# Kernel tuning notes

Measured on AMD Instinct MI355X. Metric: run time of the kernel, lower is better.

Reference implementation:

```python
import jax, jax.numpy as jnp
import numpy as np

B, N, C = 16, 2048, 512
NUM_HEADS = 8
D = C // NUM_HEADS  # 64


def setup_inputs() -> dict:
    key = jax.random.key(0)
    ks = jax.random.split(key, 8)
    s = 0.02
    return {
        "x": jax.random.normal(ks[0], (B, N, C), dtype=jnp.float32),
        "Wq": jax.random.normal(ks[1], (D, C), dtype=jnp.float32) * s,
        "bq": jax.random.normal(ks[2], (D,), dtype=jnp.float32) * s,
        "Wk": jax.random.normal(ks[3], (D, C), dtype=jnp.float32) * s,
        "bk": jax.random.normal(ks[4], (D,), dtype=jnp.float32) * s,
        "Wv": jax.random.normal(ks[5], (C, C), dtype=jnp.float32) * s,
        "bv": jax.random.normal(ks[6], (C,), dtype=jnp.float32) * s,
        "gamma": jax.random.normal(ks[7], (1,), dtype=jnp.float32) * 0.1,
    }


def reference(x, Wq, bq, Wk, bk, Wv, bv, gamma):
    # x: [B, N, C]; torch code permutes to [B, C, N] (channels for Conv1d)
    xt = jnp.transpose(x, (0, 2, 1))                      # [B, C, N]
    # 1x1 Conv1d == pointwise linear over channel dim
    q = jnp.einsum('dc,bcn->bdn', Wq, xt) + bq[None, :, None]   # [B, D, N]
    k = jnp.einsum('dc,bcn->bdn', Wk, xt) + bk[None, :, None]   # [B, D, N]
    v = jnp.einsum('oc,bcn->bon', Wv, xt) + bv[None, :, None]   # [B, C, N]
    # energy[b, n, m] = <q[:, n], k[:, m]>
    energy = jnp.einsum('bdn,bdm->bnm', q, k)             # [B, N, N]
    attention = jax.nn.softmax(energy, axis=-1)           # [B, N, N]
    # out = bmm(v, attention^T): out[b, c, n] = sum_m v[b, c, m] * attn[b, n, m]
    out = jnp.einsum('bcm,bnm->bcn', v, attention)        # [B, C, N]
    out = gamma[0] * out + xt
    return jnp.transpose(out, (0, 2, 1))                  # [B, N, C]
```

## Files before the change

### kernel.cpp

```cpp
#include <hip/hip_runtime.h>
#include <hip/hip_bf16.h>

typedef __bf16 bf16x8 __attribute__((ext_vector_type(8)));
typedef float f32x4 __attribute__((ext_vector_type(4)));

#define B_ 16
#define N_ 2048
#define C_ 512
#define D_ 64

__device__ __forceinline__ float bf2f(ushort u) {
    union { uint i; float f; } w; w.i = ((uint)u) << 16; return w.f;
}
__device__ __forceinline__ ushort f2bf(float f) {
    union { float f; uint i; } w; w.f = f;
    uint u = w.i;
    u = (u + 0x7fffu + ((u >> 16) & 1u)) >> 16;
    return (ushort)u;
}
__device__ __forceinline__ __bf16 u2b(ushort u) {
    union { ushort s; __bf16 b; } w; w.s = u; return w.b;
}
__device__ __forceinline__ bf16x8 ld8u(const ushort* p) { return *(const bf16x8*)p; }
__device__ __forceinline__ bf16x8 ld8f(const float* p) {
    f32x4 a = *(const f32x4*)p;
    f32x4 b = *(const f32x4*)(p + 4);
    bf16x8 r;
    r[0] = u2b(f2bf(a[0])); r[1] = u2b(f2bf(a[1]));
    r[2] = u2b(f2bf(a[2])); r[3] = u2b(f2bf(a[3]));
    r[4] = u2b(f2bf(b[0])); r[5] = u2b(f2bf(b[1]));
    r[6] = u2b(f2bf(b[2])); r[7] = u2b(f2bf(b[3]));
    return r;
}

__device__ __forceinline__ void gload16(const ushort* g, ushort* l) {
    __builtin_amdgcn_global_load_lds(
        (const __attribute__((address_space(1))) void*)g,
        (__attribute__((address_space(3))) void*)l, 16, 0, 0);
}

__global__ void probe_kernel(const void* x, int* flag) {
    int lane = threadIdx.x & 63;
    ushort u = ((const ushort*)x)[lane * 2];
    float v = fabsf(bf2f(u));
    bool sane = (v > 9.3e-10f) && (v < 1.1e9f) && (v == v);
    unsigned long long m = __ballot(sane);
    if (threadIdx.x == 0) *flag = (__popcll(m) >= 48) ? 0 : 1;
}

__launch_bounds__(256, 2)
__global__ void proj_qk_kernel(const void* __restrict__ X,
                               const void* __restrict__ Wq_,
                               const void* __restrict__ bq_,
                               const void* __restrict__ Wk_,
                               const void* __restrict__ bk_,
                               ushort* __restrict__ outq,
                               ushort* __restrict__ outk,
                               const int* __restrict__ flag) {
    const int isf32 = *flag;
    const ushort* Xu  = (const ushort*)X;
    const float*  Xf  = (const float*)X;
    const ushort* Wqu = (const ushort*)Wq_;
    const float*  Wqf = (const float*)Wq_;
    const ushort* Wku = (const ushort*)Wk_;
    const float*  Wkf = (const float*)Wk_;
    const ushort* Bqu = (const ushort*)bq_;
    const float*  Bqf = (const float*)bq_;
    const ushort* Bku = (const ushort*)bk_;
    const float*  Bkf = (const float*)bk_;

    __shared__ ushort lA[64][72];
    __shared__ ushort lBq[64][72];
    __shared__ ushort lBk[64][72];
    const int tid  = threadIdx.x;
    const int wave = tid >> 6, lane = tid & 63;
    const int quad = lane >> 4, li = lane & 15;
    const int m0 = blockIdx.x * 64;

    f32x4 accq[4], acck[4];
    #pragma unroll
    for (int t = 0; t < 4; ++t) {
        accq[t] = (f32x4){0.f, 0.f, 0.f, 0.f};
        acck[t] = (f32x4){0.f, 0.f, 0.f, 0.f};
    }

    for (int k0 = 0; k0 < C_; k0 += 64) {
        __syncthreads();
        #pragma unroll
        for (int it = 0; it < 2; ++it) {
            int idx = tid + it * 256;
            int row = idx >> 3, seg = idx & 7;
            size_t ea = (size_t)(m0 + row) * C_ + k0 + seg * 8;
            size_t eb = (size_t)row * C_ + k0 + seg * 8;
            if (!isf32) {
                *(bf16x8*)&lA[row][seg * 8]  = ld8u(Xu + ea);
                *(bf16x8*)&lBq[row][seg * 8] = ld8u(Wqu + eb);
                *(bf16x8*)&lBk[row][seg * 8] = ld8u(Wku + eb);
            } else {
                *(bf16x8*)&lA[row][seg * 8]  = ld8f(Xf + ea);
                *(bf16x8*)&lBq[row][seg * 8] = ld8f(Wqf + eb);
                *(bf16x8*)&lBk[row][seg * 8] = ld8f(Wkf + eb);
            }
        }
        __syncthreads();
        #pragma unroll
        for (int ks = 0; ks < 2; ++ks) {
            bf16x8 a = *(const bf16x8*)&lA[wave * 16 + li][ks * 32 + quad * 8];
            #pragma unroll
            for (int t = 0; t < 4; ++t) {
                bf16x8 bq8 = *(const bf16x8*)&lBq[t * 16 + li][ks * 32 + quad * 8];
                bf16x8 bk8 = *(const bf16x8*)&lBk[t * 16 + li][ks * 32 + quad * 8];
                accq[t] = __builtin_amdgcn_mfma_f32_16x16x32_bf16(a, bq8, accq[t], 0, 0, 0);
                acck[t] = __builtin_amdgcn_mfma_f32_16x16x32_bf16(a, bk8, acck[t], 0, 0, 0);
            }
        }
    }

    #pragma unroll
    for (int t = 0; t < 4; ++t) {
        int c = t * 16 + li;
        float bvq = isf32 ? Bqf[c] : bf2f(Bqu[c]);
        float bvk = isf32 ? Bkf[c] : bf2f(Bku[c]);
        #pragma unroll
        for (int j = 0; j < 4; ++j) {
            int m = m0 + wave * 16 + quad * 4 + j;
            outq[(size_t)m * D_ + c] = f2bf(accq[t][j] + bvq);
            outk[(size_t)m * D_ + c] = f2bf(acck[t][j] + bvk);
        }
    }
}

template<int NCOLS, int MODE>
__launch_bounds__(256, 2)
__global__ void proj_kernel(const void* __restrict__ X,
                            const void* __restrict__ W,
                            const void* __restrict__ bias,
                            ushort* __restrict__ out,
                            const int* __restrict__ flag,
                            size_t xoff) {
    const int isf32 = *flag;
    const ushort* Xu = (const ushort*)X + xoff;
    const float*  Xf = (const float*)X + xoff;
    const ushort* Wu = (const ushort*)W;
    const float*  Wf = (const float*)W;
    const ushort* Bu = (const ushort*)bias;
    const float*  Bf = (const float*)bias;

    __shared__ ushort lA[64][72];
    __shared__ ushort lB[64][72];
    const int tid  = threadIdx.x;
    const int wave = tid >> 6, lane = tid & 63;
    const int quad = lane >> 4, li = lane & 15;
    const int m0 = blockIdx.x * 64;
    const int n0 = blockIdx.y * 64;

    f32x4 acc[4];
    #pragma unroll
    for (int t = 0; t < 4; ++t) acc[t] = (f32x4){0.f, 0.f, 0.f, 0.f};

    for (int k0 = 0; k0 < C_; k0 += 64) {
        __syncthreads();
        #pragma unroll
        for (int it = 0; it < 2; ++it) {
            int idx = tid + it * 256;
            int row = idx >> 3, seg = idx & 7;
            size_t ea = (size_t)(m0 + row) * C_ + k0 + seg * 8;
            size_t eb = (size_t)(n0 + row) * C_ + k0 + seg * 8;
            if (!isf32) {
                *(bf16x8*)&lA[row][seg * 8] = ld8u(Xu + ea);
                *(bf16x8*)&lB[row][seg * 8] = ld8u(Wu + eb);
            } else {
                *(bf16x8*)&lA[row][seg * 8] = ld8f(Xf + ea);
                *(bf16x8*)&lB[row][seg * 8] = ld8f(Wf + eb);
            }
        }
        __syncthreads();
        #pragma unroll
        for (int ks = 0; ks < 2; ++ks) {
            bf16x8 a = *(const bf16x8*)&lA[wave * 16 + li][ks * 32 + quad * 8];
            #pragma unroll
            for (int t = 0; t < 4; ++t) {
                bf16x8 b = *(const bf16x8*)&lB[t * 16 + li][ks * 32 + quad * 8];
                acc[t] = __builtin_amdgcn_mfma_f32_16x16x32_bf16(a, b, acc[t], 0, 0, 0);
            }
        }
    }

    #pragma unroll
    for (int t = 0; t < 4; ++t) {
        int c = n0 + t * 16 + li;
        float bv = isf32 ? Bf[c] : bf2f(Bu[c]);
        if (MODE == 0) {
            #pragma unroll
            for (int j = 0; j < 4; ++j) {
                int m = m0 + wave * 16 + quad * 4 + j;
                out[(size_t)m * NCOLS + c] = f2bf(acc[t][j] + bv);
            }
        } else {
            int m = m0 + wave * 16 + quad * 4;
            int b = m >> 11, ml = m & (N_ - 1);
            ushort4 pk;
            pk.x = f2bf(acc[t][0] + bv);
            pk.y = f2bf(acc[t][1] + bv);
            pk.z = f2bf(acc[t][2] + bv);
            pk.w = f2bf(acc[t][3] + bv);
            *(ushort4*)(out + ((size_t)(b * C_ + c)) * N_ + ml) = pk;
        }
    }
}

__launch_bounds__(512, 4)
__global__ void attn_fused(const ushort* __restrict__ q,
                           const ushort* __restrict__ kk,
                           const ushort* __restrict__ vt,
                           const void* __restrict__ x,
                           const void* __restrict__ gptr,
                           void* __restrict__ out,
                           const int* __restrict__ flag) {
    __shared__ ushort Vl[2][256 * 64];
    __shared__ ushort Pl[64 * 64];
    __shared__ float  ll[64];

    const int tid  = threadIdx.x;
    const int wave = tid >> 6, lane = tid & 63;
    const int quad = lane >> 4, li = lane & 15;
    const int wq = wave & 1;
    const int wm = wave >> 1;
    const int b  = blockIdx.z;
    const int q0 = blockIdx.x * 64;
    const int c0 = blockIdx.y * 256;

    const ushort* kb = kk + (size_t)b * N_ * D_;
    const ushort* vb = vt + ((size_t)b * C_ + c0) * N_;

    const int lrow8 = lane >> 3;
    const int lseg  = (lane & 7) ^ lrow8;

    bf16x8 qf[2][2];
    #pragma unroll
    for (int i = 0; i < 2; ++i)
        #pragma unroll
        for (int ks = 0; ks < 2; ++ks)
            qf[i][ks] = ld8u(q + ((size_t)(b * N_ + q0 + wq * 32 + i * 16 + li)) * D_
                               + ks * 32 + quad * 8);

    f32x4 acc[2][4];
    #pragma unroll
    for (int i = 0; i < 2; ++i)
        #pragma unroll
        for (int j = 0; j < 4; ++j) acc[i][j] = (f32x4){0.f, 0.f, 0.f, 0.f};

    f32x4 accp[2];
    float s4[2][4];
    #pragma unroll
    for (int i = 0; i < 2; ++i) {
        accp[i] = (f32x4){0.f, 0.f, 0.f, 0.f};
        #pragma unroll
        for (int j = 0; j < 4; ++j) s4[i][j] = 0.f;
    }

    #pragma unroll
    for (int it = 0; it < 4; ++it) {
        int rbase = wave * 32 + it * 8;
        gload16(vb + (size_t)(rbase + lrow8) * N_ + lseg * 8, &Vl[0][rbase * 64]);
    }
    {
        bf16x8 k0 = ld8u(kb + (size_t)(wm * 16 + li) * D_ + quad * 8);
        bf16x8 k1 = ld8u(kb + (size_t)(wm * 16 + li) * D_ + 32 + quad * 8);
        accp[0] = __builtin_amdgcn_mfma_f32_16x16x32_bf16(qf[0][0], k0, accp[0], 0, 0, 0);
        accp[1] = __builtin_amdgcn_mfma_f32_16x16x32_bf16(qf[1][0], k0, accp[1], 0, 0, 0);
        accp[0] = __builtin_amdgcn_mfma_f32_16x16x32_bf16(qf[0][1], k1, accp[0], 0, 0, 0);
        accp[1] = __builtin_amdgcn_mfma_f32_16x16x32_bf16(qf[1][1], k1, accp[1], 0, 0, 0);
    }
    bf16x8 kreg0 = ld8u(kb + (size_t)(64 + wm * 16 + li) * D_ + quad * 8);
    bf16x8 kreg1 = ld8u(kb + (size_t)(64 + wm * 16 + li) * D_ + 32 + quad * 8);

    for (int t = 0; t < 32; ++t) {
        const int cur = t & 1;
        if (t < 31) {
            #pragma unroll
            for (int it = 0; it < 4; ++it) {
                int rbase = wave * 32 + it * 8;
                gload16(vb + (size_t)(rbase + lrow8) * N_ + (t + 1) * 64 + lseg * 8,
                        &Vl[cur ^ 1][rbase * 64]);
            }
        }
        #pragma unroll
        for (int i = 0; i < 2; ++i)
            #pragma unroll
            for (int j = 0; j < 4; ++j) {
                int r = wq * 32 + i * 16 + quad * 4 + j;
                int m = wm * 16 + li;
                float e = __expf(fminf(accp[i][j], 60.f));
                s4[i][j] += e;
                *(__bf16*)&Pl[r * 64 + (((m >> 3) ^ (r & 7)) * 8) + (m & 7)] = (__bf16)e;
            }
        if (t < 31) {
            f32x4 np0 = (f32x4){0.f, 0.f, 0.f, 0.f};
            f32x4 np1 = (f32x4){0.f, 0.f, 0.f, 0.f};
            np0 = __builtin_amdgcn_mfma_f32_16x16x32_bf16(qf[0][0], kreg0, np0, 0, 0, 0);
            np1 = __builtin_amdgcn_mfma_f32_16x16x32_bf16(qf[1][0], kreg0, np1, 0, 0, 0);
            np0 = __builtin_amdgcn_mfma_f32_16x16x32_bf16(qf[0][1], kreg1, np0, 0, 0, 0);
            np1 = __builtin_amdgcn_mfma_f32_16x16x32_bf16(qf[1][1], kreg1, np1, 0, 0, 0);
            if (t < 30) {
                kreg0 = ld8u(kb + (size_t)((t + 2) * 64 + wm * 16 + li) * D_ + quad * 8);
                kreg1 = ld8u(kb + (size_t)((t + 2) * 64 + wm * 16 + li) * D_ + 32 + quad * 8);
            }
            accp[0] = np0;
            accp[1] = np1;
        }
        if (t < 30)       asm volatile("s_waitcnt vmcnt(6) lgkmcnt(0)" ::: "memory");
        else if (t == 30) asm volatile("s_waitcnt vmcnt(4) lgkmcnt(0)" ::: "memory");
        else              asm volatile("s_waitcnt vmcnt(0) lgkmcnt(0)" ::: "memory");
        __builtin_amdgcn_sched_barrier(0);
        __builtin_amdgcn_s_barrier();
        __builtin_amdgcn_sched_barrier(0);

        __builtin_amdgcn_s_setprio(1);
        #pragma unroll
        for (int ks = 0; ks < 2; ++ks) {
            bf16x8 af[2];
            #pragma unroll
            for (int i = 0; i < 2; ++i)
                af[i] = *(const bf16x8*)&Pl[(wq * 32 + i * 16 + li) * 64
                                            + (((ks * 4 + quad) ^ (li & 7)) * 8)];
            #pragma unroll
            for (int j = 0; j < 4; ++j) {
                bf16x8 vf = *(const bf16x8*)&Vl[cur][(wm * 64 + j * 16 + li) * 64
                                                    + (((ks * 4 + quad) ^ (li & 7)) * 8)];
                #pragma unroll
                for (int i = 0; i < 2; ++i)
                    acc[i][j] = __builtin_amdgcn_mfma_f32_16x16x32_bf16(
                        af[i], vf, acc[i][j], 0, 0, 0);
            }
        }
        __builtin_amdgcn_s_setprio(0);

        __builtin_amdgcn_sched_barrier(0);
        __builtin_amdgcn_s_barrier();
        __builtin_amdgcn_sched_barrier(0);
    }

    __syncthreads();
    if (tid < 64) ll[tid] = 0.f;
    __syncthreads();
    #pragma unroll
    for (int i = 0; i < 2; ++i)
        #pragma unroll
        for (int j = 0; j < 4; ++j) {
            float s = s4[i][j];
            s += __shfl_xor(s, 1, 64);
            s += __shfl_xor(s, 2, 64);
            s += __shfl_xor(s, 4, 64);
            s += __shfl_xor(s, 8, 64);
            if (li == 0) atomicAdd(&ll[wq * 32 + i * 16 + quad * 4 + j], s);
        }
    __syncthreads();

    const int isf32 = *flag;
    const float g = isf32 ? ((const float*)gptr)[0] : bf2f(((const ushort*)gptr)[0]);
    const ushort* xu = (const ushort*)x;
    const float*  xf = (const float*)x;
    ushort* ou = (ushort*)out;
    float*  of = (float*)out;
    #pragma unroll
    for (int i = 0; i < 2; ++i)
        #pragma unroll
        for (int jj = 0; jj < 4; ++jj) {
            int nl = wq * 32 + i * 16 + quad * 4 + jj;
            float inv = 1.f / ll[nl];
            size_t rowb = ((size_t)(b * N_ + q0 + nl)) * C_;
            #pragma unroll
            for (int j = 0; j < 4; ++j) {
                int cg = c0 + wm * 64 + j * 16 + li;
                size_t idx = rowb + cg;
                float xv  = isf32 ? xf[idx] : bf2f(xu[idx]);
                float val = g * (acc[i][j][jj] * inv) + xv;
                if (isf32) of[idx] = val; else ou[idx] = f2bf(val);
            }
        }
}

extern "C" void kernel_launch(void* const* d_in, const int* in_sizes, int n_in,
                              void* d_out, int out_size, void* d_ws, size_t ws_size,
                              hipStream_t stream) {
    (void)in_sizes; (void)n_in; (void)out_size; (void)ws_size;
    const void* x     = d_in[0];
    const void* Wq    = d_in[1];
    const void* bq    = d_in[2];
    const void* Wk    = d_in[3];
    const void* bk    = d_in[4];
    const void* Wv    = d_in[5];
    const void* bv    = d_in[6];
    const void* gamma = d_in[7];

    int*    flag = (int*)d_ws;
    ushort* q    = (ushort*)((char*)d_ws + 256);
    ushort* kk   = q  + (size_t)B_ * N_ * D_;
    ushort* vt   = kk + (size_t)B_ * N_ * D_;

    probe_kernel<<<1, 64, 0, stream>>>(x, flag);

    const int M = B_ * N_;
    proj_qk_kernel<<<dim3(M / 64), 256, 0, stream>>>(x, Wq, bq, Wk, bk, q, kk, flag);
    proj_kernel<C_, 1><<<dim3(M / 64, C_ / 64), 256, 0, stream>>>(
        x, Wv, bv, vt, flag, 0);
    attn_fused<<<dim3(N_ / 64, 2, B_), 512, 0, stream>>>(
        q, kk, vt, x, gamma, d_out, flag);
}
```

Before: 330.1 us.

## Merge Q/K/V projections into one 128x128-tiled GEMM kernel

Replaces the separate QK and V projection kernels with a single GEMM over the concatenated 640-column weight (Wq|Wk|Wv). Each block now computes a 128x128 tile with 2x2 waves and 4x4 MFMA fragments per wave, so each A and B fragment loaded from LDS is reused more often, and x is read fewer times overall. The epilogue sends each column to the q, k or transposed v output. In exchange it uses more registers and LDS per block, adds per-row branches in the weight-load address selection, and the q/k stores stay scalar and uncoalesced.

```diff
diff --git a/kernel.cpp b/kernel.cpp
--- a/kernel.cpp
+++ b/kernel.cpp
@@ -49,162 +49,108 @@
 }
 
 __launch_bounds__(256, 2)
-__global__ void proj_qk_kernel(const void* __restrict__ X,
-                               const void* __restrict__ Wq_,
-                               const void* __restrict__ bq_,
-                               const void* __restrict__ Wk_,
-                               const void* __restrict__ bk_,
-                               ushort* __restrict__ outq,
-                               ushort* __restrict__ outk,
-                               const int* __restrict__ flag) {
+__global__ void proj_all(const void* __restrict__ X,
+                         const void* __restrict__ Wq_, const void* __restrict__ bq_,
+                         const void* __restrict__ Wk_, const void* __restrict__ bk_,
+                         const void* __restrict__ Wv_, const void* __restrict__ bv_,
+                         ushort* __restrict__ outq,
+                         ushort* __restrict__ outk,
+                         ushort* __restrict__ outv,
+                         const int* __restrict__ flag) {
     const int isf32 = *flag;
-    const ushort* Xu  = (const ushort*)X;
-    const float*  Xf  = (const float*)X;
-    const ushort* Wqu = (const ushort*)Wq_;
-    const float*  Wqf = (const float*)Wq_;
-    const ushort* Wku = (const ushort*)Wk_;
-    const float*  Wkf = (const float*)Wk_;
-    const ushort* Bqu = (const ushort*)bq_;
-    const float*  Bqf = (const float*)bq_;
-    const ushort* Bku = (const ushort*)bk_;
-    const float*  Bkf = (const float*)bk_;
-
-    __shared__ ushort lA[64][72];
-    __shared__ ushort lBq[64][72];
-    __shared__ ushort lBk[64][72];
+    __shared__ ushort lA[128][72];
+    __shared__ ushort lB[128][72];
     const int tid  = threadIdx.x;
     const int wave = tid >> 6, lane = tid & 63;
     const int quad = lane >> 4, li = lane & 15;
-    const int m0 = blockIdx.x * 64;
-
-    f32x4 accq[4], acck[4];
-    #pragma unroll
-    for (int t = 0; t < 4; ++t) {
-        accq[t] = (f32x4){0.f, 0.f, 0.f, 0.f};
-        acck[t] = (f32x4){0.f, 0.f, 0.f, 0.f};
-    }
+    const int wr = (wave & 1) * 64;
+    const int wc = (wave >> 1) * 64;
+    const int m0 = blockIdx.x * 128;
+    const int n0 = blockIdx.y * 128;
+
+    f32x4 acc[4][4];
+    #pragma unroll
+    for (int i = 0; i < 4; ++i)
+        #pragma unroll
+        for (int j = 0; j < 4; ++j) acc[i][j] = (f32x4){0.f, 0.f, 0.f, 0.f};
 
     for (int k0 = 0; k0 < C_; k0 += 64) {
         __syncthreads();
         #pragma unroll
-        for (int it = 0; it < 2; ++it) {
+        for (int it = 0; it < 4; ++it) {
             int idx = tid + it * 256;
             int row = idx >> 3, seg = idx & 7;
+            int n = n0 + row;
             size_t ea = (size_t)(m0 + row) * C_ + k0 + seg * 8;
-            size_t eb = (size_t)row * C_ + k0 + seg * 8;
             if (!isf32) {
-                *(bf16x8*)&lA[row][seg * 8]  = ld8u(Xu + ea);
-                *(bf16x8*)&lBq[row][seg * 8] = ld8u(Wqu + eb);
-                *(bf16x8*)&lBk[row][seg * 8] = ld8u(Wku + eb);
+                const ushort* bs = (n < 64)  ? (const ushort*)Wq_ + (size_t)n * C_
+                                 : (n < 128) ? (const ushort*)Wk_ + (size_t)(n - 64) * C_
+                                             : (const ushort*)Wv_ + (size_t)(n - 128) * C_;
+                *(bf16x8*)&lA[row][seg * 8] = ld8u((const ushort*)X + ea);
+                *(bf16x8*)&lB[row][seg * 8] = ld8u(bs + k0 + seg * 8);
             } else {
-                *(bf16x8*)&lA[row][seg * 8]  = ld8f(Xf + ea);
-                *(bf16x8*)&lBq[row][seg * 8] = ld8f(Wqf + eb);
-                *(bf16x8*)&lBk[row][seg * 8] = ld8f(Wkf + eb);
+                const float* bs = (n < 64)  ? (const float*)Wq_ + (size_t)n * C_
+                                : (n < 128) ? (const float*)Wk_ + (size_t)(n - 64) * C_
+                                            : (const float*)Wv_ + (size_t)(n - 128) * C_;
+                *(bf16x8*)&lA[row][seg * 8] = ld8f((const float*)X + ea);
+                *(bf16x8*)&lB[row][seg * 8] = ld8f(bs + k0 + seg * 8);
             }
         }
         __syncthreads();
         #pragma unroll
         for (int ks = 0; ks < 2; ++ks) {
-            bf16x8 a = *(const bf16x8*)&lA[wave * 16 + li][ks * 32 + quad * 8];
-            #pragma unroll
-            for (int t = 0; t < 4; ++t) {
-                bf16x8 bq8 = *(const bf16x8*)&lBq[t * 16 + li][ks * 32 + quad * 8];
-                bf16x8 bk8 = *(const bf16x8*)&lBk[t * 16 + li][ks * 32 + quad * 8];
-                accq[t] = __builtin_amdgcn_mfma_f32_16x16x32_bf16(a, bq8, accq[t], 0, 0, 0);
-                acck[t] = __builtin_amdgcn_mfma_f32_16x16x32_bf16(a, bk8, acck[t], 0, 0, 0);
-            }
-        }
-    }
-
-    #pragma unroll
-    for (int t = 0; t < 4; ++t) {
-        int c = t * 16 + li;
-        float bvq = isf32 ? Bqf[c] : bf2f(Bqu[c]);
-        float bvk = isf32 ? Bkf[c] : bf2f(Bku[c]);
-        #pragma unroll
-        for (int j = 0; j < 4; ++j) {
-            int m = m0 + wave * 16 + quad * 4 + j;
-            outq[(size_t)m * D_ + c] = f2bf(accq[t][j] + bvq);
-            outk[(size_t)m * D_ + c] = f2bf(acck[t][j] + bvk);
-        }
-    }
-}
-
-template<int NCOLS, int MODE>
-__launch_bounds__(256, 2)
-__global__ void proj_kernel(const void* __restrict__ X,
-                            const void* __restrict__ W,
-                            const void* __restrict__ bias,
-                            ushort* __restrict__ out,
-                            const int* __restrict__ flag,
-                            size_t xoff) {
-    const int isf32 = *flag;
-    const ushort* Xu = (const ushort*)X + xoff;
-    const float*  Xf = (const float*)X + xoff;
-    const ushort* Wu = (const ushort*)W;
-    const float*  Wf = (const float*)W;
-    const ushort* Bu = (const ushort*)bias;
-    const float*  Bf = (const float*)bias;
-
-    __shared__ ushort lA[64][72];
-    __shared__ ushort lB[64][72];
-    const int tid  = threadIdx.x;
-    const int wave = tid >> 6, lane = tid & 63;
-    const int quad = lane >> 4, li = lane & 15;
-    const int m0 = blockIdx.x * 64;
-    const int n0 = blockIdx.y * 64;
-
-    f32x4 acc[4];
-    #pragma unroll
-    for (int t = 0; t < 4; ++t) acc[t] = (f32x4){0.f, 0.f, 0.f, 0.f};
-
-    for (int k0 = 0; k0 < C_; k0 += 64) {
-        __syncthreads();
-        #pragma unroll
-        for (int it = 0; it < 2; ++it) {
-            int idx = tid + it * 256;
-            int row = idx >> 3, seg = idx & 7;
-            size_t ea = (size_t)(m0 + row) * C_ + k0 + seg * 8;
-            size_t eb = (size_t)(n0 + row) * C_ + k0 + seg * 8;
-            if (!isf32) {
-                *(bf16x8*)&lA[row][seg * 8] = ld8u(Xu + ea);
-                *(bf16x8*)&lB[row][seg * 8] = ld8u(Wu + eb);
-            } else {
-                *(bf16x8*)&lA[row][seg * 8] = ld8f(Xf + ea);
-                *(bf16x8*)&lB[row][seg * 8] = ld8f(Wf + eb);
-            }
-        }
-        __syncthreads();
-        #pragma unroll
-        for (int ks = 0; ks < 2; ++ks) {
-            bf16x8 a = *(const bf16x8*)&lA[wave * 16 + li][ks * 32 + quad * 8];
-            #pragma unroll
-            for (int t = 0; t < 4; ++t) {
-                bf16x8 b = *(const bf16x8*)&lB[t * 16 + li][ks * 32 + quad * 8];
-                acc[t] = __builtin_amdgcn_mfma_f32_16x16x32_bf16(a, b, acc[t], 0, 0, 0);
-            }
-        }
-    }
-
-    #pragma unroll
-    for (int t = 0; t < 4; ++t) {
-        int c = n0 + t * 16 + li;
-        float bv = isf32 ? Bf[c] : bf2f(Bu[c]);
-        if (MODE == 0) {
-            #pragma unroll
-            for (int j = 0; j < 4; ++j) {
-                int m = m0 + wave * 16 + quad * 4 + j;
-                out[(size_t)m * NCOLS + c] = f2bf(acc[t][j] + bv);
-            }
+            bf16x8 af[4], bfr[4];
+            #pragma unroll
+            for (int i = 0; i < 4; ++i)
+                af[i] = *(const bf16x8*)&lA[wr + i * 16 + li][ks * 32 + quad * 8];
+            #pragma unroll
+            for (int j = 0; j < 4; ++j)
+                bfr[j] = *(const bf16x8*)&lB[wc + j * 16 + li][ks * 32 + quad * 8];
+            #pragma unroll
+            for (int i = 0; i < 4; ++i)
+                #pragma unroll
+                for (int j = 0; j < 4; ++j)
+                    acc[i][j] = __builtin_amdgcn_mfma_f32_16x16x32_bf16(
+                        af[i], bfr[j], acc[i][j], 0, 0, 0);
+        }
+    }
+
+    #pragma unroll
+    for (int j2 = 0; j2 < 4; ++j2) {
+        int c = n0 + wc + j2 * 16 + li;
+        float bv;
+        if (!isf32) {
+            bv = (c < 64)  ? bf2f(((const ushort*)bq_)[c])
+               : (c < 128) ? bf2f(((const ushort*)bk_)[c - 64])
+                           : bf2f(((const ushort*)bv_)[c - 128]);
         } else {
-            int m = m0 + wave * 16 + quad * 4;
-            int b = m >> 11, ml = m & (N_ - 1);
-            ushort4 pk;
-            pk.x = f2bf(acc[t][0] + bv);
-            pk.y = f2bf(acc[t][1] + bv);
-            pk.z = f2bf(acc[t][2] + bv);
-            pk.w = f2bf(acc[t][3] + bv);
-            *(ushort4*)(out + ((size_t)(b * C_ + c)) * N_ + ml) = pk;
+            bv = (c < 64)  ? ((const float*)bq_)[c]
+               : (c < 128) ? ((const float*)bk_)[c - 64]
+                           : ((const float*)bv_)[c - 128];
+        }
+        if (c < 128) {
+            ushort* dst = (c < 64) ? outq : outk;
+            int cl = c & 63;
+            #pragma unroll
+            for (int i = 0; i < 4; ++i)
+                #pragma unroll
+                for (int j = 0; j < 4; ++j) {
+                    int m = m0 + wr + i * 16 + quad * 4 + j;
+                    dst[(size_t)m * D_ + cl] = f2bf(acc[i][j2][j] + bv);
+                }
+        } else {
+            int cv = c - 128;
+            #pragma unroll
+            for (int i = 0; i < 4; ++i) {
+                int m = m0 + wr + i * 16 + quad * 4;
+                int b = m >> 11, ml = m & (N_ - 1);
+                ushort4 pk;
+                pk.x = f2bf(acc[i][j2][0] + bv);
+                pk.y = f2bf(acc[i][j2][1] + bv);
+                pk.z = f2bf(acc[i][j2][2] + bv);
+                pk.w = f2bf(acc[i][j2][3] + bv);
+                *(ushort4*)(outv + ((size_t)(b * C_ + cv)) * N_ + ml) = pk;
+            }
         }
     }
 }
@@ -401,10 +347,9 @@
 
     probe_kernel<<<1, 64, 0, stream>>>(x, flag);
 
-    const int M = B_ * N_;
-    proj_qk_kernel<<<dim3(M / 64), 256, 0, stream>>>(x, Wq, bq, Wk, bk, q, kk, flag);
-    proj_kernel<C_, 1><<<dim3(M / 64, C_ / 64), 256, 0, stream>>>(
-        x, Wv, bv, vt, flag, 0);
+    proj_all<<<dim3(B_ * N_ / 128, 640 / 128), 256, 0, stream>>>(
+        x, Wq, bq, Wk, bk, Wv, bv, q, kk, vt, flag);
+
     attn_fused<<<dim3(N_ / 64, 2, B_), 512, 0, stream>>>(
         q, kk, vt, x, gamma, d_out, flag);
 }
```

After: 303.8 us. 8.0% less time.
